# Kernel tuning notes

Measured on AMD Instinct MI355X. Metric: run time of the kernel, lower is better.

## Reference

```python
import jax, jax.numpy as jnp
import numpy as np

BS = 16          # scenes per batch
N_POINTS = 500_000  # points per scene
N_OBJ = 16       # distinct instance tags; all present w.h.p. so n_obj = max+1 = N_OBJ


def setup_inputs() -> dict:
    key = jax.random.key(0)
    k1, k2 = jax.random.split(key)
    pc = jax.random.normal(k1, (BS, N_POINTS, 3), dtype=jnp.float32)
    node_tag = jax.random.randint(k2, (BS, N_POINTS), 0, N_OBJ)
    return {"pc": pc, "node_tag": node_tag}


def _relabel_row(tags):
    # torch: for i, tag in enumerate(tags.unique()): out[tags==tag] = i
    # == rank of each tag among the sorted distinct tags present in this row
    present = jnp.zeros((N_OBJ,), jnp.int32).at[tags].set(1)
    ranks = jnp.cumsum(present) - 1  # dense id per original tag value
    return ranks[tags]


def _encode_keypoints(pc, node_tag):
    bs, n_pts, _ = pc.shape
    obj_node_tag = jax.vmap(_relabel_row)(node_tag)          # (bs, n_pts)
    n_obj = N_OBJ                                            # obj_node_tag.max()+1 (static)
    batch_offset = jnp.arange(bs, dtype=obj_node_tag.dtype)[:, None] * n_obj
    obj_batch = obj_node_tag + batch_offset                  # (bs, n_pts) global segment ids

    flat_pc = pc.reshape(-1, 3)
    seg = obj_batch.reshape(-1)
    nseg = bs * n_obj
    mins = jax.ops.segment_min(flat_pc, seg, num_segments=nseg)   # (bs*n_obj, 3)
    maxs = jax.ops.segment_max(flat_pc, seg, num_segments=nseg)
    counts = jax.ops.segment_sum(jnp.ones((flat_pc.shape[0],), jnp.float32), seg, num_segments=nseg)
    nonempty = (counts > 0)[:, None]
    mins = jnp.where(nonempty, mins, 0.0)  # torch code leaves empty objects at 0
    maxs = jnp.where(nonempty, maxs, 0.0)

    mins = mins.reshape(bs, n_obj, 3)
    maxs = maxs.reshape(bs, n_obj, 3)
    # interleave: bbox[b, 2i] = min_i, bbox[b, 2i+1] = max_i
    bbox = jnp.stack([mins, maxs], axis=2).reshape(bs, 2 * n_obj, 3)
    # faithful to torch .view(bs, 2, n_obj, 3).mean(dim=1) row-major split
    barycenter = bbox.reshape(bs, 2, n_obj, 3).mean(axis=1)       # (bs, n_obj, 3)
    keypoints = jnp.concatenate([bbox, barycenter], axis=1)       # (bs, 3*n_obj, 3)
    return keypoints, obj_batch


def reference(pc, node_tag):
    return _encode_keypoints(pc, node_tag)
```

## Files before the change

kernel.cpp:

```cpp
#include <hip/hip_runtime.h>

#define BS 16
#define NP 500000
#define NQ (NP / 4)
#define NOBJ 16
#define NSEG3 48
#define GX 128
#define NSUB 16

typedef float f32x4 __attribute__((ext_vector_type(4)));

#define WS_SMAX 98304
#define WS_SMSK 196608

__device__ __forceinline__ unsigned fkey(float f) {
    unsigned u = __float_as_uint(f);
    return (u & 0x80000000u) ? ~u : (u | 0x80000000u);
}
__device__ __forceinline__ float keyf(unsigned k) {
    unsigned u = (k & 0x80000000u) ? (k ^ 0x80000000u) : ~k;
    return __uint_as_float(u);
}

__global__ __launch_bounds__(256) void kmain(const float* __restrict__ pc,
                                             const int* __restrict__ tag,
                                             unsigned* __restrict__ ws,
                                             float* __restrict__ out) {
    __shared__ unsigned lmin[NSUB * NSEG3], lmax[NSUB * NSEG3];
    __shared__ unsigned lmask;
    const int b = blockIdx.y, x = blockIdx.x, tid = threadIdx.x;
    if (tid == 0) lmask = 0u;
    for (int j = tid; j < NSUB * NSEG3; j += 256) { lmin[j] = 0xFFFFFFFFu; lmax[j] = 0u; }
    __syncthreads();

    const int sub = tid & (NSUB - 1);
    const float fb = (float)(b * NOBJ);
    const int4*   tag4 = (const int4*)(tag + (size_t)b * NP);
    const float4* pc4  = (const float4*)(pc + (size_t)b * NP * 3);
    f32x4* out4 = (f32x4*)(out + 2304 + (size_t)b * NP);
    unsigned m = 0u;
    for (int i = x * 256 + tid; i < NQ; i += GX * 256) {
        int4 t = tag4[i];
        float4 f0 = pc4[i * 3 + 0];
        float4 f1 = pc4[i * 3 + 1];
        float4 f2 = pc4[i * 3 + 2];
        f32x4 ob = {fb + (float)t.x, fb + (float)t.y, fb + (float)t.z, fb + (float)t.w};
        __builtin_nontemporal_store(ob, &out4[i]);
        m |= (1u << t.x) | (1u << t.y) | (1u << t.z) | (1u << t.w);
        int a0 = t.x * 48 + sub, a1 = t.y * 48 + sub, a2 = t.z * 48 + sub, a3 = t.w * 48 + sub;
        unsigned k;
        k = fkey(f0.x); atomicMin(&lmin[a0 +  0], k); atomicMax(&lmax[a0 +  0], k);
        k = fkey(f0.y); atomicMin(&lmin[a0 + 16], k); atomicMax(&lmax[a0 + 16], k);
        k = fkey(f0.z); atomicMin(&lmin[a0 + 32], k); atomicMax(&lmax[a0 + 32], k);
        k = fkey(f0.w); atomicMin(&lmin[a1 +  0], k); atomicMax(&lmax[a1 +  0], k);
        k = fkey(f1.x); atomicMin(&lmin[a1 + 16], k); atomicMax(&lmax[a1 + 16], k);
        k = fkey(f1.y); atomicMin(&lmin[a1 + 32], k); atomicMax(&lmax[a1 + 32], k);
        k = fkey(f1.z); atomicMin(&lmin[a2 +  0], k); atomicMax(&lmax[a2 +  0], k);
        k = fkey(f1.w); atomicMin(&lmin[a2 + 16], k); atomicMax(&lmax[a2 + 16], k);
        k = fkey(f2.x); atomicMin(&lmin[a2 + 32], k); atomicMax(&lmax[a2 + 32], k);
        k = fkey(f2.y); atomicMin(&lmin[a3 +  0], k); atomicMax(&lmax[a3 +  0], k);
        k = fkey(f2.z); atomicMin(&lmin[a3 + 16], k); atomicMax(&lmax[a3 + 16], k);
        k = fkey(f2.w); atomicMin(&lmin[a3 + 32], k); atomicMax(&lmax[a3 + 32], k);
    }
    atomicOr(&lmask, m);
    __syncthreads();

    const int slot = b * GX + x;
    if (tid < NSEG3) {
        unsigned mn = 0xFFFFFFFFu, mx = 0u;
        #pragma unroll
        for (int s = 0; s < NSUB; ++s) {
            mn = min(mn, lmin[tid * NSUB + s]);
            mx = max(mx, lmax[tid * NSUB + s]);
        }
        ws[slot * NSEG3 + tid] = mn;
        ws[WS_SMAX + slot * NSEG3 + tid] = mx;
    }
    if (tid == 0) ws[WS_SMSK + slot] = lmask;
}

__global__ __launch_bounds__(256) void k3(const unsigned* __restrict__ ws,
                                          float* __restrict__ out) {
    __shared__ unsigned pmin[4][NSEG3], pmax[4][NSEG3];
    __shared__ unsigned smin[NSEG3], smax[NSEG3];
    __shared__ unsigned smask;
    __shared__ float lut[NOBJ];
    const int b = blockIdx.x, tid = threadIdx.x;
    const int wave = tid >> 6, lane = tid & 63;

    if (tid == 0) smask = 0u;
    __syncthreads();

    if (lane < NSEG3) {
        unsigned mn = 0xFFFFFFFFu, mx = 0u;
        const int x0 = wave * (GX / 4);
        #pragma unroll 8
        for (int x2 = x0; x2 < x0 + GX / 4; ++x2) {
            mn = min(mn, ws[(b * GX + x2) * NSEG3 + lane]);
            mx = max(mx, ws[WS_SMAX + (b * GX + x2) * NSEG3 + lane]);
        }
        pmin[wave][lane] = mn;
        pmax[wave][lane] = mx;
    } else if (lane >= 56) {
        const int base = b * GX + wave * (GX / 4) + (lane - 56) * 4;
        unsigned mm = ws[WS_SMSK + base] | ws[WS_SMSK + base + 1]
                    | ws[WS_SMSK + base + 2] | ws[WS_SMSK + base + 3];
        atomicOr(&smask, mm);
    }
    __syncthreads();

    if (tid < NSEG3)
        smin[tid] = min(min(pmin[0][tid], pmin[1][tid]), min(pmin[2][tid], pmin[3][tid]));
    else if (tid >= 64 && tid < 64 + NSEG3) {
        const int e = tid - 64;
        smax[e] = max(max(pmax[0][e], pmax[1][e]), max(pmax[2][e], pmax[3][e]));
    }
    __syncthreads();
    const unsigned mask = smask;

    if (tid == 0) {
        int tag_of[NOBJ];
        int r = -1;
        for (int t = 0; t < NOBJ; ++t)
            if ((mask >> t) & 1u) { ++r; tag_of[r] = t; }
        int nd = r + 1;
        float bbox[32][3];
        for (int i = 0; i < NOBJ; ++i) {
            for (int c = 0; c < 3; ++c) {
                float mn = 0.f, mx = 0.f;
                if (i < nd) {
                    int t = tag_of[i];
                    mn = keyf(smin[t * 3 + c]);
                    mx = keyf(smax[t * 3 + c]);
                }
                bbox[2 * i][c] = mn;
                bbox[2 * i + 1][c] = mx;
            }
        }
        float* ob = out + (size_t)b * 48 * 3;
        for (int j = 0; j < 32; ++j)
            for (int c = 0; c < 3; ++c)
                ob[j * 3 + c] = bbox[j][c];
        for (int j = 0; j < 16; ++j)
            for (int c = 0; c < 3; ++c)
                ob[(32 + j) * 3 + c] = 0.5f * (bbox[j][c] + bbox[16 + j][c]);
    }

    if (mask != 0xFFFFu) {
        if (tid < NOBJ)
            lut[tid] = (float)(__popc(mask & ((2u << tid) - 1u)) - 1 + b * NOBJ);
        __syncthreads();
        const float fb = (float)(b * NOBJ);
        float4* out4 = (float4*)(out + 2304 + (size_t)b * NP);
        for (int i = tid; i < NQ; i += 256) {
            float4 v = out4[i];
            out4[i] = make_float4(lut[(int)(v.x - fb)], lut[(int)(v.y - fb)],
                                  lut[(int)(v.z - fb)], lut[(int)(v.w - fb)]);
        }
    }
}

extern "C" void kernel_launch(void* const* d_in, const int* in_sizes, int n_in,
                              void* d_out, int out_size, void* d_ws, size_t ws_size,
                              hipStream_t stream) {
    const float* pc  = (const float*)d_in[0];
    const int*   tag = (const int*)d_in[1];
    float* out = (float*)d_out;
    unsigned* ws = (unsigned*)d_ws;

    kmain<<<dim3(GX, BS), 256, 0, stream>>>(pc, tag, ws, out);
    k3<<<BS, 256, 0, stream>>>(ws, out);
}
```

Before: 39.30 us.

## Issue all loads per wave upfront with fixed per-wave chunk instead of grid-stride loop

Replaces the grid-stride loop with a fixed assignment of 256 quads per wave, where each lane issues four independent tag loads and twelve pc loads before doing any atomics. This raises memory-level parallelism so load latency overlaps, instead of serialising load-then-atomics per iteration. Adds launch_bounds occupancy hint (4 blocks per CU). Coverage depends on GX*4*256 >= NQ (128*1024 = 131072 >= 125000), which holds, though more registers are needed.

```diff
diff --git a/kernel.cpp b/kernel.cpp
--- a/kernel.cpp
+++ b/kernel.cpp
@@ -7,6 +7,7 @@
 #define NSEG3 48
 #define GX 128
 #define NSUB 16
+#define WQ 256
 
 typedef float f32x4 __attribute__((ext_vector_type(4)));
 
@@ -22,10 +23,34 @@
     return __uint_as_float(u);
 }
 
-__global__ __launch_bounds__(256) void kmain(const float* __restrict__ pc,
-                                             const int* __restrict__ tag,
-                                             unsigned* __restrict__ ws,
-                                             float* __restrict__ out) {
+#define ATOMS(T, F0, F1, F2) do {                                                   \
+    int a0_ = (T).x * 48 + sub, a1_ = (T).y * 48 + sub;                             \
+    int a2_ = (T).z * 48 + sub, a3_ = (T).w * 48 + sub;                             \
+    unsigned k_;                                                                     \
+    k_ = fkey((F0).x); atomicMin(&lmin[a0_ +  0], k_); atomicMax(&lmax[a0_ +  0], k_); \
+    k_ = fkey((F0).y); atomicMin(&lmin[a0_ + 16], k_); atomicMax(&lmax[a0_ + 16], k_); \
+    k_ = fkey((F0).z); atomicMin(&lmin[a0_ + 32], k_); atomicMax(&lmax[a0_ + 32], k_); \
+    k_ = fkey((F0).w); atomicMin(&lmin[a1_ +  0], k_); atomicMax(&lmax[a1_ +  0], k_); \
+    k_ = fkey((F1).x); atomicMin(&lmin[a1_ + 16], k_); atomicMax(&lmax[a1_ + 16], k_); \
+    k_ = fkey((F1).y); atomicMin(&lmin[a1_ + 32], k_); atomicMax(&lmax[a1_ + 32], k_); \
+    k_ = fkey((F1).z); atomicMin(&lmin[a2_ +  0], k_); atomicMax(&lmax[a2_ +  0], k_); \
+    k_ = fkey((F1).w); atomicMin(&lmin[a2_ + 16], k_); atomicMax(&lmax[a2_ + 16], k_); \
+    k_ = fkey((F2).x); atomicMin(&lmin[a2_ + 32], k_); atomicMax(&lmax[a2_ + 32], k_); \
+    k_ = fkey((F2).y); atomicMin(&lmin[a3_ +  0], k_); atomicMax(&lmax[a3_ +  0], k_); \
+    k_ = fkey((F2).z); atomicMin(&lmin[a3_ + 16], k_); atomicMax(&lmax[a3_ + 16], k_); \
+    k_ = fkey((F2).w); atomicMin(&lmin[a3_ + 32], k_); atomicMax(&lmax[a3_ + 32], k_); \
+} while (0)
+
+#define EMIT(T, Q) do {                                                              \
+    f32x4 ob_ = {fb + (float)(T).x, fb + (float)(T).y, fb + (float)(T).z, fb + (float)(T).w}; \
+    __builtin_nontemporal_store(ob_, &out4[Q]);                                      \
+    m |= (1u << (T).x) | (1u << (T).y) | (1u << (T).z) | (1u << (T).w);              \
+} while (0)
+
+__global__ __launch_bounds__(256, 4) void kmain(const float* __restrict__ pc,
+                                                const int* __restrict__ tag,
+                                                unsigned* __restrict__ ws,
+                                                float* __restrict__ out) {
     __shared__ unsigned lmin[NSUB * NSEG3], lmax[NSUB * NSEG3];
     __shared__ unsigned lmask;
     const int b = blockIdx.y, x = blockIdx.x, tid = threadIdx.x;
@@ -33,34 +58,32 @@
     for (int j = tid; j < NSUB * NSEG3; j += 256) { lmin[j] = 0xFFFFFFFFu; lmax[j] = 0u; }
     __syncthreads();
 
-    const int sub = tid & (NSUB - 1);
+    const int sub  = tid & (NSUB - 1);
+    const int lane = tid & 63;
+    const int wv   = x * 4 + (tid >> 6);
     const float fb = (float)(b * NOBJ);
     const int4*   tag4 = (const int4*)(tag + (size_t)b * NP);
     const float4* pc4  = (const float4*)(pc + (size_t)b * NP * 3);
     f32x4* out4 = (f32x4*)(out + 2304 + (size_t)b * NP);
     unsigned m = 0u;
-    for (int i = x * 256 + tid; i < NQ; i += GX * 256) {
-        int4 t = tag4[i];
-        float4 f0 = pc4[i * 3 + 0];
-        float4 f1 = pc4[i * 3 + 1];
-        float4 f2 = pc4[i * 3 + 2];
-        f32x4 ob = {fb + (float)t.x, fb + (float)t.y, fb + (float)t.z, fb + (float)t.w};
-        __builtin_nontemporal_store(ob, &out4[i]);
-        m |= (1u << t.x) | (1u << t.y) | (1u << t.z) | (1u << t.w);
-        int a0 = t.x * 48 + sub, a1 = t.y * 48 + sub, a2 = t.z * 48 + sub, a3 = t.w * 48 + sub;
-        unsigned k;
-        k = fkey(f0.x); atomicMin(&lmin[a0 +  0], k); atomicMax(&lmax[a0 +  0], k);
-        k = fkey(f0.y); atomicMin(&lmin[a0 + 16], k); atomicMax(&lmax[a0 + 16], k);
-        k = fkey(f0.z); atomicMin(&lmin[a0 + 32], k); atomicMax(&lmax[a0 + 32], k);
-        k = fkey(f0.w); atomicMin(&lmin[a1 +  0], k); atomicMax(&lmax[a1 +  0], k);
-        k = fkey(f1.x); atomicMin(&lmin[a1 + 16], k); atomicMax(&lmax[a1 + 16], k);
-        k = fkey(f1.y); atomicMin(&lmin[a1 + 32], k); atomicMax(&lmax[a1 + 32], k);
-        k = fkey(f1.z); atomicMin(&lmin[a2 +  0], k); atomicMax(&lmax[a2 +  0], k);
-        k = fkey(f1.w); atomicMin(&lmin[a2 + 16], k); atomicMax(&lmax[a2 + 16], k);
-        k = fkey(f2.x); atomicMin(&lmin[a2 + 32], k); atomicMax(&lmax[a2 + 32], k);
-        k = fkey(f2.y); atomicMin(&lmin[a3 +  0], k); atomicMax(&lmax[a3 +  0], k);
-        k = fkey(f2.z); atomicMin(&lmin[a3 + 16], k); atomicMax(&lmax[a3 + 16], k);
-        k = fkey(f2.w); atomicMin(&lmin[a3 + 32], k); atomicMax(&lmax[a3 + 32], k);
+
+    const int q0 = wv * WQ + lane;
+    if (q0 < NQ) {
+        const bool v1 = (q0 + 64 < NQ), v2 = (q0 + 128 < NQ), v3 = (q0 + 192 < NQ);
+        const int  q1 = v1 ? q0 + 64 : q0;
+        const int  q2 = v2 ? q0 + 128 : q0;
+        const int  q3 = v3 ? q0 + 192 : q0;
+
+        int4 t0 = tag4[q0], t1 = tag4[q1], t2 = tag4[q2], t3 = tag4[q3];
+        float4 a0 = pc4[3 * q0 + 0], a1 = pc4[3 * q0 + 1], a2 = pc4[3 * q0 + 2];
+        float4 b0 = pc4[3 * q1 + 0], b1 = pc4[3 * q1 + 1], b2 = pc4[3 * q1 + 2];
+        float4 c0 = pc4[3 * q2 + 0], c1 = pc4[3 * q2 + 1], c2 = pc4[3 * q2 + 2];
+        float4 d0 = pc4[3 * q3 + 0], d1 = pc4[3 * q3 + 1], d2 = pc4[3 * q3 + 2];
+
+        EMIT(t0, q0); ATOMS(t0, a0, a1, a2);
+        if (v1) { EMIT(t1, q1); ATOMS(t1, b0, b1, b2); }
+        if (v2) { EMIT(t2, q2); ATOMS(t2, c0, c1, c2); }
+        if (v3) { EMIT(t3, q3); ATOMS(t3, d0, d1, d2); }
     }
     atomicOr(&lmask, m);
     __syncthreads();
```

Result: no change. 39.07 us (median of 2 runs) (-0.6%).
